# Performance work log

Measured on AMD Instinct MI355X. Metric: run time of the kernel, lower is better.

Reference implementation:

```python
import jax, jax.numpy as jnp
import numpy as np
from jax import lax

VOCAB = 32000
D_MODEL = 768
N_LAYERS = 2
D_STATE = 16
EXPAND = 2
D_CONV = 4
DT_RANK = 48
D_INNER = EXPAND * D_MODEL
B, L = 2, 1024
EPS = 1e-5


def rmsnorm(x, w):
    return x * lax.rsqrt(jnp.mean(x * x, axis=-1, keepdims=True) + EPS) * w


def selective_scan(deltaA, deltaBx, C):
    # deltaA, deltaBx: (B, L, ED, N); C: (B, L, N)
    h0 = jnp.zeros((deltaA.shape[0], deltaA.shape[2], deltaA.shape[3]), deltaA.dtype)

    def step(h, inp):
        dA, dBx, c = inp
        h = dA * h + dBx                      # (B, ED, N)
        y = jnp.einsum('ben,bn->be', h, c)    # (B, ED)
        return h, y

    xs = (deltaA.transpose(1, 0, 2, 3), deltaBx.transpose(1, 0, 2, 3), C.transpose(1, 0, 2))
    _, ys = lax.scan(step, h0, xs)            # (L, B, ED)
    return ys.transpose(1, 0, 2)


def mamba_block(x, in_w, conv_w, conv_b, xproj_w, dt_w, dt_b, A_log, Dp, out_w):
    # x: (B, L, D)
    xz = jnp.einsum('bld,ed->ble', x, in_w)               # (B, L, 2*ED)
    xa, z = jnp.split(xz, 2, axis=-1)
    # depthwise causal conv over time
    xc = xa.transpose(0, 2, 1)                            # (B, ED, L)
    kern = conv_w[:, None, :]                             # (ED, 1, d_conv)
    xc = lax.conv_general_dilated(xc, kern, (1,), [(D_CONV - 1, 0)],
                                  dimension_numbers=('NCH', 'OIH', 'NCH'),
                                  feature_group_count=D_INNER)
    xa = jax.nn.silu((xc + conv_b[None, :, None]).transpose(0, 2, 1))  # (B, L, ED)
    # ssm params
    dbc = jnp.einsum('ble,re->blr', xa, xproj_w)          # (B, L, dt_rank+2N)
    delta, Bm, Cm = jnp.split(dbc, [DT_RANK, DT_RANK + D_STATE], axis=-1)
    delta = jax.nn.softplus(jnp.einsum('blr,er->ble', delta, dt_w) + dt_b)  # (B, L, ED)
    A = -jnp.exp(A_log)                                   # (ED, N)
    deltaA = jnp.exp(delta[..., None] * A)                # (B, L, ED, N)
    deltaBx = delta[..., None] * Bm[:, :, None, :] * xa[..., None]
    y = selective_scan(deltaA, deltaBx, Cm) + Dp * xa     # (B, L, ED)
    y = y * jax.nn.silu(z)
    return jnp.einsum('ble,de->bld', y, out_w)            # (B, L, D)


def setup_inputs() -> dict:
    key = jax.random.key(0)
    ks = jax.random.split(key, 16)
    s = 0.02
    inp = {}
    inp['x'] = jax.random.randint(ks[0], (B, L), 0, VOCAB)
    inp['embed_W'] = jax.random.normal(ks[1], (VOCAB, D_MODEL), jnp.float32) * s
    inp['norm_w'] = jnp.ones((N_LAYERS, D_MODEL), jnp.float32)
    inp['in_proj_w'] = jax.random.normal(ks[2], (N_LAYERS, 2 * D_INNER, D_MODEL), jnp.float32) * s
    inp['conv_w'] = jax.random.normal(ks[3], (N_LAYERS, D_INNER, D_CONV), jnp.float32) * 0.2
    inp['conv_b'] = jnp.zeros((N_LAYERS, D_INNER), jnp.float32)
    inp['x_proj_w'] = jax.random.normal(ks[4], (N_LAYERS, DT_RANK + 2 * D_STATE, D_INNER), jnp.float32) * s
    inp['dt_proj_w'] = jax.random.normal(ks[5], (N_LAYERS, D_INNER, DT_RANK), jnp.float32) * (DT_RANK ** -0.5)
    inp['dt_proj_b'] = jnp.log(jnp.expm1(jnp.full((N_LAYERS, D_INNER), 0.01, jnp.float32)))
    inp['A_log'] = jnp.log(jnp.broadcast_to(jnp.arange(1, D_STATE + 1, dtype=jnp.float32), (N_LAYERS, D_INNER, D_STATE)))
    inp['D_param'] = jnp.ones((N_LAYERS, D_INNER), jnp.float32)
    inp['out_proj_w'] = jax.random.normal(ks[6], (N_LAYERS, D_MODEL, D_INNER), jnp.float32) * s
    inp['normf_w'] = jnp.ones((D_MODEL,), jnp.float32)
    inp['head_w'] = jax.random.normal(ks[7], (VOCAB, D_MODEL), jnp.float32) * s
    inp['head_b'] = jnp.zeros((VOCAB,), jnp.float32)
    return inp


def reference(x, embed_W, norm_w, in_proj_w, conv_w, conv_b, x_proj_w,
              dt_proj_w, dt_proj_b, A_log, D_param, out_proj_w,
              normf_w, head_w, head_b):
    h = embed_W[x]                                        # (B, L, D)
    for i in range(N_LAYERS):
        h = h + mamba_block(rmsnorm(h, norm_w[i]), in_proj_w[i], conv_w[i],
                            conv_b[i], x_proj_w[i], dt_proj_w[i], dt_proj_b[i],
                            A_log[i], D_param[i], out_proj_w[i])
    h = rmsnorm(h, normf_w)
    logits = jnp.einsum('bld,vd->blv', h, head_w) + head_b
    return logits
```

## Files before the change

kernel.cpp:

```cpp
#include <hip/hip_runtime.h>
#include <cmath>

constexpr int DM     = 768;
constexpr int DI     = 1536;
constexpr int DI2    = 3072;
constexpr int DSTATE = 16;
constexpr int DTRANK = 48;
constexpr int NDBC   = 80;
constexpr int BB     = 2;
constexpr int LL     = 1024;
constexpr int NT     = BB * LL;
constexpr int NVOCAB = 32000;
constexpr float EPSF = 1e-5f;

constexpr int NC = 32;
constexpr int CL = LL / NC;

typedef unsigned short ushort_t;
typedef __bf16 bf16x8 __attribute__((ext_vector_type(8)));
typedef float  f32x4  __attribute__((ext_vector_type(4)));

__device__ inline ushort_t f2bf(float x) {
    unsigned int u = __builtin_bit_cast(unsigned int, x);
    unsigned int r = (u + 0x7FFFu + ((u >> 16) & 1u)) >> 16;
    return (ushort_t)r;
}

__global__ __launch_bounds__(256) void f2b_kernel(const float* __restrict__ in,
                                                  ushort_t* __restrict__ out, int n4) {
    int i = blockIdx.x * blockDim.x + threadIdx.x;
    if (i >= n4) return;
    float4 v = ((const float4*)in)[i];
    ushort4 o;
    o.x = f2bf(v.x); o.y = f2bf(v.y); o.z = f2bf(v.z); o.w = f2bf(v.w);
    ((ushort4*)out)[i] = o;
}

__global__ void embed_kernel(const int* __restrict__ x, const float* __restrict__ W,
                             float* __restrict__ h) {
    int t = blockIdx.x;
    int row = x[t];
    const float4* src = (const float4*)(W + (size_t)row * DM);
    float4* dst = (float4*)(h + (size_t)t * DM);
    for (int i = threadIdx.x; i < DM / 4; i += blockDim.x) dst[i] = src[i];
}

__global__ __launch_bounds__(256) void rmsnorm_kernel(const float* __restrict__ x,
                                                      const float* __restrict__ w,
                                                      ushort_t* __restrict__ o) {
    int t = blockIdx.x;
    const float* xr = x + (size_t)t * DM;
    float s = 0.f;
    for (int i = threadIdx.x; i < DM; i += 256) { float v = xr[i]; s += v * v; }
    #pragma unroll
    for (int off = 32; off >= 1; off >>= 1) s += __shfl_down(s, off, 64);
    __shared__ float wsum[4];
    if ((threadIdx.x & 63) == 0) wsum[threadIdx.x >> 6] = s;
    __syncthreads();
    float tot = wsum[0] + wsum[1] + wsum[2] + wsum[3];
    float r = rsqrtf(tot / DM + EPSF);
    ushort_t* orow = o + (size_t)t * DM;
    for (int i = threadIdx.x; i < DM; i += 256) orow[i] = f2bf(xr[i] * r * w[i]);
}

__device__ inline void gl_lds16(const void* g, void* l) {
    auto gp = (const __attribute__((address_space(1))) void*)(unsigned long long)(uintptr_t)g;
    auto lp = (__attribute__((address_space(3))) void*)(unsigned int)(uintptr_t)l;
    __builtin_amdgcn_global_load_lds(gp, lp, 16, 0, 0);
}

__global__ __launch_bounds__(256) void bgemm_bt(const ushort_t* __restrict__ A, int lda,
                                                const ushort_t* __restrict__ W, int ldw,
                                                float* __restrict__ C, int ldc,
                                                int K,
                                                const float* __restrict__ bias,
                                                const float* __restrict__ resid) {
    __shared__ ushort_t As[4][128 * 32];
    __shared__ ushort_t Bs[4][128 * 32];

    const int GX  = gridDim.x;
    const int nwg = GX * gridDim.y;
    int orig = blockIdx.y * GX + blockIdx.x;
    int q = nwg >> 3, r = nwg & 7, xcd = orig & 7, lq = orig >> 3;
    int wg = (xcd < r ? xcd * (q + 1) : r * (q + 1) + (xcd - r) * q) + lq;
    const int m0 = (wg % GX) * 128;
    const int n0 = (wg / GX) * 128;

    const int wave = threadIdx.x >> 6;
    const int lane = threadIdx.x & 63;
    const int lrow = lane >> 2;

    f32x4 acc[4][4] = {};

    const ushort_t* Ab = A + (size_t)m0 * lda;
    const ushort_t* Wb = W + (size_t)n0 * ldw;
    const int wm = (wave >> 1) * 64;
    const int wn = (wave & 1) * 64;

    auto stage = [&](int buf, int k0) {
        #pragma unroll
        for (int rr = 0; rr < 2; ++rr) {
            const int rowbase = rr * 64 + wave * 16;
            const int row = rowbase + lrow;
            const int csw = (((lane & 3) ^ ((row >> 1) & 3)) << 3);
            gl_lds16(Ab + (size_t)row * lda + k0 + csw, (char*)As[buf] + rowbase * 64);
            gl_lds16(Wb + (size_t)row * ldw + k0 + csw, (char*)Bs[buf] + rowbase * 64);
        }
    };

    const int S = K >> 5;
    stage(0, 0);
    if (S > 1) stage(1, 32);
    if (S > 2) stage(2, 64);

    const int rsw = ((lane >> 1) & 3);
    for (int s = 0; s < S; ++s) {
        const int ahead = S - 1 - s;
        if (ahead >= 2)      asm volatile("s_waitcnt vmcnt(8)" ::: "memory");
        else if (ahead == 1) asm volatile("s_waitcnt vmcnt(4)" ::: "memory");
        else                 asm volatile("s_waitcnt vmcnt(0)" ::: "memory");
        __builtin_amdgcn_s_barrier();
        if (s + 3 < S) stage((s + 3) & 3, (s + 3) << 5);

        const int cur = s & 3;
        bf16x8 af[4], bfr[4];
        const int rchunk = (((lane >> 4) ^ rsw) << 4);
        #pragma unroll
        for (int i = 0; i < 4; ++i) {
            af[i]  = *(const bf16x8*)((char*)As[cur] + (wm + i * 16 + (lane & 15)) * 64 + rchunk);
            bfr[i] = *(const bf16x8*)((char*)Bs[cur] + (wn + i * 16 + (lane & 15)) * 64 + rchunk);
        }
        __builtin_amdgcn_s_setprio(1);
        #pragma unroll
        for (int i = 0; i < 4; ++i)
            #pragma unroll
            for (int j = 0; j < 4; ++j)
                acc[i][j] = __builtin_amdgcn_mfma_f32_16x16x32_bf16(af[i], bfr[j], acc[i][j], 0, 0, 0);
        __builtin_amdgcn_s_setprio(0);
    }

    const int cn = lane & 15;
    const int cr = (lane >> 4) * 4;
    #pragma unroll
    for (int i = 0; i < 4; ++i) {
        #pragma unroll
        for (int j = 0; j < 4; ++j) {
            const int col = n0 + wn + j * 16 + cn;
            const float bv = bias ? bias[col] : 0.f;
            #pragma unroll
            for (int rr = 0; rr < 4; ++rr) {
                const int row = m0 + wm + i * 16 + cr + rr;
                const size_t idx = (size_t)row * ldc + col;
                float v = acc[i][j][rr] + bv;
                if (resid) v += resid[idx];
                C[idx] = v;
            }
        }
    }
}

constexpr int BM = 64, BN = 64, BK = 16;
__global__ __launch_bounds__(256) void sgemm_bt(const float* __restrict__ A, int lda,
                                                const float* __restrict__ W, int ldw,
                                                float* __restrict__ C, int ldc,
                                                int M, int N, int K,
                                                const float* __restrict__ bias,
                                                const float* __restrict__ resid,
                                                int act) {
    __shared__ float As[BK][BM];
    __shared__ float Ws[BK][BN];
    const int m0 = blockIdx.x * BM;
    const int n0 = blockIdx.y * BN;
    const int nz = gridDim.z;
    const int Kc = K / nz;
    const int kbeg = blockIdx.z * Kc;
    const int kend = kbeg + Kc;
    const int tid = threadIdx.x;
    const int tn = tid & 15, tm = tid >> 4;
    const int lr = tid >> 2;
    const int lk = (tid & 3) * 4;

    float acc[4][4] = {};

    for (int k0 = kbeg; k0 < kend; k0 += BK) {
        {
            float4 v = *(const float4*)(A + (size_t)(m0 + lr) * lda + k0 + lk);
            As[lk + 0][lr] = v.x; As[lk + 1][lr] = v.y;
            As[lk + 2][lr] = v.z; As[lk + 3][lr] = v.w;
            int n = n0 + lr;
            float4 u = make_float4(0.f, 0.f, 0.f, 0.f);
            if (n < N) u = *(const float4*)(W + (size_t)n * ldw + k0 + lk);
            Ws[lk + 0][lr] = u.x; Ws[lk + 1][lr] = u.y;
            Ws[lk + 2][lr] = u.z; Ws[lk + 3][lr] = u.w;
        }
        __syncthreads();
        #pragma unroll
        for (int kk = 0; kk < BK; ++kk) {
            float4 a = *(const float4*)&As[kk][tm * 4];
            float4 w = *(const float4*)&Ws[kk][tn * 4];
            acc[0][0] += a.x * w.x; acc[0][1] += a.x * w.y; acc[0][2] += a.x * w.z; acc[0][3] += a.x * w.w;
            acc[1][0] += a.y * w.x; acc[1][1] += a.y * w.y; acc[1][2] += a.y * w.z; acc[1][3] += a.y * w.w;
            acc[2][0] += a.z * w.x; acc[2][1] += a.z * w.y; acc[2][2] += a.z * w.z; acc[2][3] += a.z * w.w;
            acc[3][0] += a.w * w.x; acc[3][1] += a.w * w.y; acc[3][2] += a.w * w.z; acc[3][3] += a.w * w.w;
        }
        __syncthreads();
    }

    #pragma unroll
    for (int i = 0; i < 4; ++i) {
        int m = m0 + tm * 4 + i;
        #pragma unroll
        for (int j = 0; j < 4; ++j) {
            int n = n0 + tn * 4 + j;
            if (n < N) {
                const size_t idx = (size_t)m * ldc + n;
                float v = acc[i][j];
                if (nz > 1) {
                    atomicAdd(&C[idx], v);
                } else {
                    if (bias)  v += bias[n];
                    if (resid) v += resid[idx];
                    if (act == 1) v = (v > 20.f) ? v : log1pf(expf(v));
                    C[idx] = v;
                }
            }
        }
    }
}

__global__ void conv_silu_kernel(const float* __restrict__ xz, const float* __restrict__ cw,
                                 const float* __restrict__ cb, float* __restrict__ xa,
                                 float* __restrict__ dbc0) {
    int idx = blockIdx.x * blockDim.x + threadIdx.x;
    if (idx < NT * NDBC) dbc0[idx] = 0.f;
    if (idx >= NT * DI) return;
    int e = idx % DI;
    int t = idx / DI;
    int l = t & (LL - 1);
    float acc = cb[e];
    #pragma unroll
    for (int k = 0; k < 4; ++k) {
        int ll = l - 3 + k;
        if (ll >= 0) acc += cw[e * 4 + k] * xz[(size_t)(t - 3 + k) * DI2 + e];
    }
    xa[idx] = acc / (1.f + expf(-acc));
}


__global__ __launch_bounds__(256) void scan_carry(const float* __restrict__ delta,
                                                  const float* __restrict__ xa,
                                                  const float* __restrict__ dbc,
                                                  const float* __restrict__ A_log,
                                                  float* __restrict__ Pc,
                                                  float* __restrict__ Hc) {
    const int e = blockIdx.x * 256 + threadIdx.x;
    const int c = blockIdx.y;
    const int b = blockIdx.z;
    float aen[DSTATE], h[DSTATE];
    #pragma unroll
    for (int n = 0; n < DSTATE; ++n) {
        aen[n] = -expf(A_log[e * DSTATE + n]) * 1.4426950408889634f;
        h[n] = 0.f;
    }
    float dsum = 0.f;
    const int t0 = b * LL + c * CL;
    const float* dp = delta + (size_t)t0 * DI + e;
    const float* xp = xa    + (size_t)t0 * DI + e;
    const float* bp = dbc   + (size_t)t0 * NDBC + DTRANK;
    for (int l = 0; l < CL; ++l) {
        float d  = dp[(size_t)l * DI];
        float xv = xp[(size_t)l * DI];
        const float* br = bp + (size_t)l * NDBC;
        dsum += d;
        float dxv = d * xv;
        #pragma unroll
        for (int n = 0; n < DSTATE; ++n) {
            float dA = exp2f(d * aen[n]);
            h[n] = dA * h[n] + dxv * br[n];
        }
    }
    const size_t cbase = ((size_t)(b * NC + c) * DI + e) * DSTATE;
    #pragma unroll
    for (int n = 0; n < DSTATE; ++n) {
        Pc[cbase + n] = exp2f(aen[n] * dsum);
        Hc[cbase + n] = h[n];
    }
}

__global__ __launch_bounds__(256) void scan_compose(const float* __restrict__ Pc,
                                                    float* __restrict__ Hc) {
    const int id = blockIdx.x * 256 + threadIdx.x;
    const int b = id / (DI * DSTATE);
    const int r = id - b * (DI * DSTATE);
    float cur = 0.f;
    for (int c = 0; c < NC; ++c) {
        const size_t idx = (size_t)(b * NC + c) * (DI * DSTATE) + r;
        float p  = Pc[idx];
        float hl = Hc[idx];
        Hc[idx] = cur;
        cur = p * cur + hl;
    }
}

__global__ __launch_bounds__(256) void scan_apply(const float* __restrict__ delta,
                                                  const float* __restrict__ xa,
                                                  const float* __restrict__ dbc,
                                                  const float* __restrict__ xz,
                                                  const float* __restrict__ A_log,
                                                  const float* __restrict__ Dp,
                                                  const float* __restrict__ Hc,
                                                  ushort_t* __restrict__ ys) {
    const int e = blockIdx.x * 256 + threadIdx.x;
    const int c = blockIdx.y;
    const int b = blockIdx.z;
    float aen[DSTATE], h[DSTATE];
    const size_t cbase = ((size_t)(b * NC + c) * DI + e) * DSTATE;
    #pragma unroll
    for (int n = 0; n < DSTATE; ++n) {
        aen[n] = -expf(A_log[e * DSTATE + n]) * 1.4426950408889634f;
        h[n] = Hc[cbase + n];
    }
    const float dpe = Dp[e];
    const int t0 = b * LL + c * CL;
    const float* dp = delta + (size_t)t0 * DI + e;
    const float* xp = xa    + (size_t)t0 * DI + e;
    const float* bp = dbc   + (size_t)t0 * NDBC + DTRANK;
    const float* zp = xz    + (size_t)t0 * DI2 + DI + e;
    ushort_t*    yp = ys    + (size_t)t0 * DI + e;
    for (int l = 0; l < CL; ++l) {
        float d  = dp[(size_t)l * DI];
        float xv = xp[(size_t)l * DI];
        const float* br = bp + (size_t)l * NDBC;
        const float* cr = br + DSTATE;
        float dxv = d * xv;
        float y = 0.f;
        #pragma unroll
        for (int n = 0; n < DSTATE; ++n) {
            float dA = exp2f(d * aen[n]);
            h[n] = dA * h[n] + dxv * br[n];
            y += h[n] * cr[n];
        }
        float z = zp[(size_t)l * DI2];
        float sz = z / (1.f + expf(-z));
        yp[(size_t)l * DI] = f2bf((y + dpe * xv) * sz);
    }
}

extern "C" void kernel_launch(void* const* d_in, const int* in_sizes, int n_in,
                              void* d_out, int out_size, void* d_ws, size_t ws_size,
                              hipStream_t stream) {
    const int*   x        = (const int*)  d_in[0];
    const float* embed_W  = (const float*)d_in[1];
    const float* norm_w   = (const float*)d_in[2];
    const float* in_w     = (const float*)d_in[3];
    const float* conv_w   = (const float*)d_in[4];
    const float* conv_b   = (const float*)d_in[5];
    const float* xproj_w  = (const float*)d_in[6];
    const float* dt_w     = (const float*)d_in[7];
    const float* dt_b     = (const float*)d_in[8];
    const float* A_log    = (const float*)d_in[9];
    const float* D_param  = (const float*)d_in[10];
    const float* out_w    = (const float*)d_in[11];
    const float* normf_w  = (const float*)d_in[12];
    const float* head_w   = (const float*)d_in[13];
    const float* head_b   = (const float*)d_in[14];
    float* logits = (float*)d_out;

    float* ws    = (float*)d_ws;
    float* h     = ws;
    float* xz    = h     + (size_t)NT * DM;
    float* xa    = xz    + (size_t)NT * DI2;
    float* dbc   = xa    + (size_t)NT * DI;
    float* delta = dbc   + (size_t)NT * NDBC;
    ushort_t* in_wb  = (ushort_t*)(delta + (size_t)NT * DI);
    ushort_t* out_wb = in_wb  + (size_t)2 * DI2 * DM;
    ushort_t* xnb    = out_wb + (size_t)2 * DM * DI;
    ushort_t* ys16   = xnb    + (size_t)NT * DM;
    float* Pc = (float*)(ys16 + (size_t)NT * DI);
    float* Hc = Pc + (size_t)BB * NC * DI * DSTATE;
    ushort_t* head_wb = (ushort_t*)xz;

    embed_kernel<<<NT, 192, 0, stream>>>(x, embed_W, h);

    {
        int n4 = 2 * DI2 * DM / 4;
        f2b_kernel<<<(n4 + 255) / 256, 256, 0, stream>>>(in_w, in_wb, n4);
        n4 = 2 * DM * DI / 4;
        f2b_kernel<<<(n4 + 255) / 256, 256, 0, stream>>>(out_w, out_wb, n4);
    }

    for (int i = 0; i < 2; ++i) {
        rmsnorm_kernel<<<NT, 256, 0, stream>>>(h, norm_w + (size_t)i * DM, xnb);
        bgemm_bt<<<dim3(NT / 128, DI2 / 128), 256, 0, stream>>>(
            xnb, DM, in_wb + (size_t)i * DI2 * DM, DM, xz, DI2, DM, nullptr, nullptr);
        conv_silu_kernel<<<(NT * DI + 255) / 256, 256, 0, stream>>>(
            xz, conv_w + (size_t)i * DI * 4, conv_b + (size_t)i * DI, xa, dbc);
        sgemm_bt<<<dim3(NT / BM, (NDBC + BN - 1) / BN, 8), 256, 0, stream>>>(
            xa, DI, xproj_w + (size_t)i * NDBC * DI, DI, dbc, NDBC,
            NT, NDBC, DI, nullptr, nullptr, 0);
        sgemm_bt<<<dim3(NT / BM, DI / BN), 256, 0, stream>>>(
            dbc, NDBC, dt_w + (size_t)i * DI * DTRANK, DTRANK, delta, DI,
            NT, DI, DTRANK, dt_b + (size_t)i * DI, nullptr, 1);
        scan_carry<<<dim3(DI / 256, NC, BB), 256, 0, stream>>>(
            delta, xa, dbc, A_log + (size_t)i * DI * DSTATE, Pc, Hc);
        scan_compose<<<(BB * DI * DSTATE) / 256, 256, 0, stream>>>(Pc, Hc);
        scan_apply<<<dim3(DI / 256, NC, BB), 256, 0, stream>>>(
            delta, xa, dbc, xz, A_log + (size_t)i * DI * DSTATE,
            D_param + (size_t)i * DI, Hc, ys16);
        bgemm_bt<<<dim3(NT / 128, DM / 128), 256, 0, stream>>>(
            ys16, DI, out_wb + (size_t)i * DM * DI, DI, h, DM, DI, nullptr, h);
    }

    rmsnorm_kernel<<<NT, 256, 0, stream>>>(h, normf_w, xnb);
    {
        int n4 = NVOCAB * DM / 4;
        f2b_kernel<<<(n4 + 255) / 256, 256, 0, stream>>>(head_w, head_wb, n4);
    }
    bgemm_bt<<<dim3(NT / 128, NVOCAB / 128), 256, 0, stream>>>(
        xnb, DM, head_wb, DM, logits, NVOCAB, DM, head_b, nullptr);
}
```

Measured before the change: 945.0 us.

## Double-buffer bf16 GEMM, store chunk delta sums, double scan chunk count

The bf16 GEMM drops from a 4-stage to a 2-stage LDS pipeline. Each step now waits for its LDS reads and adds a second barrier before refilling the just-consumed buffer, which cuts LDS use and may raise occupancy at the cost of less latency hiding. The chunked scan now stores only per-chunk delta sums and recomputes the decay products in the compose kernel, which shrinks the carry write traffic. The chunk count doubles, giving scan_carry and scan_apply more parallelism but making the sequential compose loop twice as long.

```diff
diff --git a/kernel.cpp b/kernel.cpp
--- a/kernel.cpp
+++ b/kernel.cpp
@@ -12,8 +12,9 @@
 constexpr int NT     = BB * LL;
 constexpr int NVOCAB = 32000;
 constexpr float EPSF = 1e-5f;
-
-constexpr int NC = 32;
+constexpr float LOG2E = 1.4426950408889634f;
+
+constexpr int NC = 64;
 constexpr int CL = LL / NC;
 
 typedef unsigned short ushort_t;
@@ -75,8 +76,8 @@
                                                 int K,
                                                 const float* __restrict__ bias,
                                                 const float* __restrict__ resid) {
-    __shared__ ushort_t As[4][128 * 32];
-    __shared__ ushort_t Bs[4][128 * 32];
+    __shared__ ushort_t As[2][128 * 32];
+    __shared__ ushort_t Bs[2][128 * 32];
 
     const int GX  = gridDim.x;
     const int nwg = GX * gridDim.y;
@@ -110,19 +111,15 @@
 
     const int S = K >> 5;
     stage(0, 0);
-    if (S > 1) stage(1, 32);
-    if (S > 2) stage(2, 64);
+    stage(1, 32);
 
     const int rsw = ((lane >> 1) & 3);
     for (int s = 0; s < S; ++s) {
-        const int ahead = S - 1 - s;
-        if (ahead >= 2)      asm volatile("s_waitcnt vmcnt(8)" ::: "memory");
-        else if (ahead == 1) asm volatile("s_waitcnt vmcnt(4)" ::: "memory");
-        else                 asm volatile("s_waitcnt vmcnt(0)" ::: "memory");
+        if (s < S - 1) asm volatile("s_waitcnt vmcnt(4)" ::: "memory");
+        else           asm volatile("s_waitcnt vmcnt(0)" ::: "memory");
         __builtin_amdgcn_s_barrier();
-        if (s + 3 < S) stage((s + 3) & 3, (s + 3) << 5);
-
-        const int cur = s & 3;
+
+        const int cur = s & 1;
         bf16x8 af[4], bfr[4];
         const int rchunk = (((lane >> 4) ^ rsw) << 4);
         #pragma unroll
@@ -130,6 +127,11 @@
             af[i]  = *(const bf16x8*)((char*)As[cur] + (wm + i * 16 + (lane & 15)) * 64 + rchunk);
             bfr[i] = *(const bf16x8*)((char*)Bs[cur] + (wn + i * 16 + (lane & 15)) * 64 + rchunk);
         }
+        asm volatile("s_waitcnt lgkmcnt(0)" ::: "memory");
+        __builtin_amdgcn_sched_barrier(0);
+        __builtin_amdgcn_s_barrier();
+        if (s + 2 < S) stage(cur, (s + 2) << 5);
+
         __builtin_amdgcn_s_setprio(1);
         #pragma unroll
         for (int i = 0; i < 4; ++i)
@@ -251,7 +253,7 @@
                                                   const float* __restrict__ xa,
                                                   const float* __restrict__ dbc,
                                                   const float* __restrict__ A_log,
-                                                  float* __restrict__ Pc,
+                                                  float* __restrict__ Ds,
                                                   float* __restrict__ Hc) {
     const int e = blockIdx.x * 256 + threadIdx.x;
     const int c = blockIdx.y;
@@ -259,7 +261,7 @@
     float aen[DSTATE], h[DSTATE];
     #pragma unroll
     for (int n = 0; n < DSTATE; ++n) {
-        aen[n] = -expf(A_log[e * DSTATE + n]) * 1.4426950408889634f;
+        aen[n] = -expf(A_log[e * DSTATE + n]) * LOG2E;
         h[n] = 0.f;
     }
     float dsum = 0.f;
@@ -281,21 +283,23 @@
     }
     const size_t cbase = ((size_t)(b * NC + c) * DI + e) * DSTATE;
     #pragma unroll
-    for (int n = 0; n < DSTATE; ++n) {
-        Pc[cbase + n] = exp2f(aen[n] * dsum);
-        Hc[cbase + n] = h[n];
-    }
-}
-
-__global__ __launch_bounds__(256) void scan_compose(const float* __restrict__ Pc,
+    for (int n = 0; n < DSTATE; ++n) Hc[cbase + n] = h[n];
+    Ds[(size_t)(b * NC + c) * DI + e] = dsum;
+}
+
+__global__ __launch_bounds__(256) void scan_compose(const float* __restrict__ Ds,
+                                                    const float* __restrict__ A_log,
                                                     float* __restrict__ Hc) {
     const int id = blockIdx.x * 256 + threadIdx.x;
     const int b = id / (DI * DSTATE);
     const int r = id - b * (DI * DSTATE);
+    const int e = r >> 4;
+    const float aen = -expf(A_log[r]) * LOG2E;
     float cur = 0.f;
     for (int c = 0; c < NC; ++c) {
-        const size_t idx = (size_t)(b * NC + c) * (DI * DSTATE) + r;
-        float p  = Pc[idx];
+        const size_t base = (size_t)(b * NC + c) * DI;
+        float p  = exp2f(aen * Ds[base + e]);
+        const size_t idx = base * DSTATE + r;
         float hl = Hc[idx];
         Hc[idx] = cur;
         cur = p * cur + hl;
@@ -317,7 +321,7 @@
     const size_t cbase = ((size_t)(b * NC + c) * DI + e) * DSTATE;
     #pragma unroll
     for (int n = 0; n < DSTATE; ++n) {
-        aen[n] = -expf(A_log[e * DSTATE + n]) * 1.4426950408889634f;
+        aen[n] = -expf(A_log[e * DSTATE + n]) * LOG2E;
         h[n] = Hc[cbase + n];
     }
     const float dpe = Dp[e];
@@ -376,8 +380,8 @@
     ushort_t* out_wb = in_wb  + (size_t)2 * DI2 * DM;
     ushort_t* xnb    = out_wb + (size_t)2 * DM * DI;
     ushort_t* ys16   = xnb    + (size_t)NT * DM;
-    float* Pc = (float*)(ys16 + (size_t)NT * DI);
-    float* Hc = Pc + (size_t)BB * NC * DI * DSTATE;
+    float* Ds = (float*)(ys16 + (size_t)NT * DI);
+    float* Hc = Ds + (size_t)BB * NC * DI;
     ushort_t* head_wb = (ushort_t*)xz;
 
     embed_kernel<<<NT, 192, 0, stream>>>(x, embed_W, h);
@@ -402,8 +406,9 @@
             dbc, NDBC, dt_w + (size_t)i * DI * DTRANK, DTRANK, delta, DI,
             NT, DI, DTRANK, dt_b + (size_t)i * DI, nullptr, 1);
         scan_carry<<<dim3(DI / 256, NC, BB), 256, 0, stream>>>(
-            delta, xa, dbc, A_log + (size_t)i * DI * DSTATE, Pc, Hc);
-        scan_compose<<<(BB * DI * DSTATE) / 256, 256, 0, stream>>>(Pc, Hc);
+            delta, xa, dbc, A_log + (size_t)i * DI * DSTATE, Ds, Hc);
+        scan_compose<<<(BB * DI * DSTATE) / 256, 256, 0, stream>>>(
+            Ds, A_log + (size_t)i * DI * DSTATE, Hc);
         scan_apply<<<dim3(DI / 256, NC, BB), 256, 0, stream>>>(
             delta, xa, dbc, xz, A_log + (size_t)i * DI * DSTATE,
             D_param + (size_t)i * DI, Hc, ys16);
```

Result: faster. 921.1 us (-2.5%).
